# Performance work log

Measured on AMD Instinct MI355X. Metric: run time of the kernel, lower is better.

The kernel has to match this reference:

```python
import jax, jax.numpy as jnp
import numpy as np

HEADS = 16
DIM_HEAD = 64
SCALE = DIM_HEAD ** (-0.5)


def setup_inputs() -> dict:
    key = jax.random.key(0)
    ks = jax.random.split(key, 6)
    B, N, D = 2, 2048, 1024
    inner = HEADS * DIM_HEAD  # 1024
    s = 0.02
    return {
        "x": jax.random.normal(ks[0], (B, N, D), dtype=jnp.float32),
        "Wq": jax.random.normal(ks[1], (D, inner), dtype=jnp.float32) * s,
        "Wk": jax.random.normal(ks[2], (D, inner), dtype=jnp.float32) * s,
        "Wv": jax.random.normal(ks[3], (D, inner), dtype=jnp.float32) * s,
        "Wo": jax.random.normal(ks[4], (inner, D), dtype=jnp.float32) * s,
        "bo": jnp.zeros((D,), dtype=jnp.float32),
    }


def reference(x, Wq, Wk, Wv, Wo, bo):
    B, N, _ = x.shape
    # projections, split heads: [B, N, inner] -> [B, H, N, d]
    def split(t):
        return t.reshape(B, N, HEADS, DIM_HEAD).transpose(0, 2, 1, 3)
    q = split(x @ Wq)
    k = split(x @ Wk)  # self-attention: context = x
    v = split(x @ Wv)
    # scores [B, H, N, N], softmax over keys
    scores = jnp.einsum('bhid,bhjd->bhij', q, k) * SCALE
    attn = jax.nn.softmax(scores, axis=-1)
    out = jnp.einsum('bhij,bhjd->bhid', attn, v)
    out = out.transpose(0, 2, 1, 3).reshape(B, N, HEADS * DIM_HEAD)
    return out @ Wo + bo
```

## Files before the change

kernel.cpp:

```cpp
#include <hip/hip_runtime.h>
#include <hip/hip_bf16.h>
#include <stdint.h>

typedef unsigned short u16;
typedef __attribute__((ext_vector_type(8))) short bf16x8;
typedef __attribute__((ext_vector_type(4))) float f32x4;
typedef __attribute__((ext_vector_type(4))) unsigned int u32x4;

#define QSCALE 0.18033688011112042f

__device__ __forceinline__ u16 f2bf(float f) {
  return __builtin_bit_cast(u16, __float2bfloat16(f));
}

__device__ __forceinline__ uint32_t pkcvt(float a, float b) {
  return (uint32_t)f2bf(a) | ((uint32_t)f2bf(b) << 16);
}

__device__ __forceinline__ void gll16(const void* g, void* l) {
  __builtin_amdgcn_global_load_lds(
      (__attribute__((address_space(1))) void*)(uintptr_t)g,
      (__attribute__((address_space(3))) void*)l, 16, 0, 0);
}

__global__ void cvt_x_kernel(const float* __restrict__ x, u16* __restrict__ xb) {
  size_t i = (size_t)blockIdx.x * 256 + threadIdx.x;
  const float4* p = (const float4*)x + i * 2;
  float4 a = p[0], b = p[1];
  ushort4 lo, hi;
  lo.x = f2bf(a.x); lo.y = f2bf(a.y); lo.z = f2bf(a.z); lo.w = f2bf(a.w);
  hi.x = f2bf(b.x); hi.y = f2bf(b.y); hi.z = f2bf(b.z); hi.w = f2bf(b.w);
  ((ushort4*)xb)[i * 2]     = lo;
  ((ushort4*)xb)[i * 2 + 1] = hi;
}

__global__ void cvt_w_kernel(const float* __restrict__ Wq, const float* __restrict__ Wk,
                             const float* __restrict__ Wv, const float* __restrict__ Wo,
                             u16* __restrict__ Wqkvt, u16* __restrict__ Wot) {
  __shared__ float tile[32][33];
  const int z = blockIdx.z;
  const float* src = (z == 0) ? Wq : (z == 1) ? Wk : (z == 2) ? Wv : Wo;
  const float scale = (z == 0) ? QSCALE : 1.0f;
  u16* dst = (z == 3) ? Wot : (Wqkvt + (size_t)z * 1024 * 1024);
  const int n0 = blockIdx.x * 32, k0 = blockIdx.y * 32;
  const int tx = threadIdx.x, ty = threadIdx.y;
#pragma unroll
  for (int i = 0; i < 4; ++i)
    tile[ty * 4 + i][tx] = src[(size_t)(k0 + ty * 4 + i) * 1024 + n0 + tx];
  __syncthreads();
#pragma unroll
  for (int i = 0; i < 4; ++i)
    dst[(size_t)(n0 + ty * 4 + i) * 1024 + k0 + tx] = f2bf(tile[tx][ty * 4 + i] * scale);
}

__global__ __launch_bounds__(256)
void gemm_qkv_kernel(const u16* __restrict__ A, const u16* __restrict__ Bt,
                     u16* __restrict__ Qb, u16* __restrict__ Kb, u16* __restrict__ Vtb) {
  __shared__ __align__(16) u16 As[128 * 32];
  __shared__ __align__(16) u16 Bs[128 * 32];
  const int row0 = blockIdx.x * 128, col0 = blockIdx.y * 128;
  const int tid = threadIdx.x, lane = tid & 63, wid = tid >> 6;
  const int wr = (wid >> 1) * 64, wc = (wid & 1) * 64;
  const int lr = lane & 15, lk = (lane >> 4) * 8;

  f32x4 acc[4][4];
#pragma unroll
  for (int m = 0; m < 4; ++m)
#pragma unroll
    for (int n = 0; n < 4; ++n) acc[m][n] = (f32x4){0.f, 0.f, 0.f, 0.f};

  const int c0 = wid * 128 + lane;

  for (int k0 = 0; k0 < 1024; k0 += 32) {
    __syncthreads();
#pragma unroll
    for (int c = 0; c < 2; ++c) {
      const int chunk = c0 + c * 64;
      const int r = chunk >> 2, kk = (chunk & 3) * 8;
      gll16(A + (size_t)(row0 + r) * 1024 + k0 + kk,
            (char*)As + (wid * 128 + c * 64) * 16);
      gll16(Bt + (size_t)(col0 + r) * 1024 + k0 + kk,
            (char*)Bs + (wid * 128 + c * 64) * 16);
    }
    __syncthreads();
    bf16x8 af[4], bfr[4];
#pragma unroll
    for (int m = 0; m < 4; ++m)
      af[m] = *(const bf16x8*)&As[(wr + m * 16 + lr) * 32 + lk];
#pragma unroll
    for (int n = 0; n < 4; ++n)
      bfr[n] = *(const bf16x8*)&Bs[(wc + n * 16 + lr) * 32 + lk];
#pragma unroll
    for (int m = 0; m < 4; ++m)
#pragma unroll
      for (int n = 0; n < 4; ++n)
        acc[m][n] = __builtin_amdgcn_mfma_f32_16x16x32_bf16(af[m], bfr[n], acc[m][n], 0, 0, 0);
  }

  const int lg = lane >> 4;
#pragma unroll
  for (int m = 0; m < 4; ++m) {
#pragma unroll
    for (int n = 0; n < 4; ++n) {
      const int gcol = col0 + wc + n * 16 + lr;
      const int w = gcol >> 10, rem = gcol & 1023;
      const int h = rem >> 6, dd = rem & 63;
      const int grow0 = row0 + wr + m * 16 + lg * 4;
      if (w == 2) {
        const int b0 = grow0 >> 11, nn0 = grow0 & 2047;
        ushort4 sv;
        sv.x = f2bf(acc[m][n][0]); sv.y = f2bf(acc[m][n][1]);
        sv.z = f2bf(acc[m][n][2]); sv.w = f2bf(acc[m][n][3]);
        *(ushort4*)&Vtb[((size_t)(b0 * 16 + h) * 64 + dd) * 2048 + nn0] = sv;
      } else {
#pragma unroll
        for (int r = 0; r < 4; ++r) {
          const int grow = grow0 + r;
          const int b = grow >> 11, nn = grow & 2047;
          const int bh = b * 16 + h;
          const u16 hv = f2bf(acc[m][n][r]);
          if (w == 0) Qb[((size_t)bh * 2048 + nn) * 64 + dd] = hv;
          else        Kb[((size_t)bh * 2048 + nn) * 64 + dd] = hv;
        }
      }
    }
  }
}

__global__ __launch_bounds__(256, 2)
void attn_kernel(const u16* __restrict__ Qb, const u16* __restrict__ Kb,
                 const u16* __restrict__ Vtb, u16* __restrict__ Ob) {
  __shared__ __align__(16) u16 Ks[2][64 * 64];
  __shared__ __align__(16) u16 Vs[2][64 * 64];
  const int tid = threadIdx.x, lane = tid & 63, wid = tid >> 6;
  const int bid = blockIdx.x;
  const int vv = (bid & 7) * 64 + (bid >> 3);
  const int qt = vv & 15, bh = vv >> 4;
  const int lr = lane & 15, lg = lane >> 4;

  const u16* Qp = Qb + ((size_t)bh * 2048 + qt * 128 + wid * 32) * 64;
  const char* Kg = (const char*)(Kb + (size_t)bh * 2048 * 64);
  const char* Vg = (const char*)(Vtb + (size_t)bh * 64 * 2048);

  bf16x8 aq[2][2];
#pragma unroll
  for (int qc = 0; qc < 2; ++qc)
#pragma unroll
    for (int ks = 0; ks < 2; ++ks)
      aq[qc][ks] = *(const bf16x8*)&Qp[(qc * 16 + lr) * 64 + ks * 32 + lg * 8];

  const int c_base = wid * 128 + lane;
  auto stage = [&](int buf, int kv0) {
#pragma unroll
    for (int i = 0; i < 2; ++i) {
      const int c = c_base + i * 64;
      const int row = c >> 3;
      const int sc = ((c & 7) * 16) ^ ((row & 7) << 4);
      gll16(Kg + (size_t)(kv0 + row) * 128 + sc, (char*)Ks[buf] + c * 16);
      gll16(Vg + (size_t)row * 4096 + kv0 * 2 + sc, (char*)Vs[buf] + c * 16);
    }
  };

  const int swz = (lr & 7) << 4;
  const int xk0 = (lg * 16) ^ swz;
  const int xk1 = (64 + lg * 16) ^ swz;

  f32x4 acco[4][2];
#pragma unroll
  for (int ct = 0; ct < 4; ++ct)
#pragma unroll
    for (int qc = 0; qc < 2; ++qc) acco[ct][qc] = (f32x4){0.f, 0.f, 0.f, 0.f};
  f32x4 lacc[2];
  lacc[0] = (f32x4){0.f, 0.f, 0.f, 0.f};
  lacc[1] = (f32x4){0.f, 0.f, 0.f, 0.f};
  const f32x4 minit = (f32x4){-8.f, -8.f, -8.f, -8.f};
  u32x4 ow;
  ow.x = ow.y = ow.z = ow.w = 0x3F803F80u;
  const bf16x8 ones = __builtin_bit_cast(bf16x8, ow);

  stage(0, 0);
  asm volatile("s_waitcnt vmcnt(0)" ::: "memory");
  __syncthreads();

  int buf = 0;
  for (int t = 0; t < 32; ++t) {
    if (t < 31) stage(buf ^ 1, (t + 1) * 64);
    const char* kbase = (const char*)Ks[buf] + lr * 128;
    const char* vbase = (const char*)Vs[buf] + lr * 128;

    bf16x8 kf[4][2];
#pragma unroll
    for (int kt = 0; kt < 4; ++kt) {
      kf[kt][0] = *(const bf16x8*)(kbase + kt * 2048 + xk0);
      kf[kt][1] = *(const bf16x8*)(kbase + kt * 2048 + xk1);
    }
    f32x4 s[4][2];
#pragma unroll
    for (int kt = 0; kt < 4; ++kt)
#pragma unroll
      for (int qc = 0; qc < 2; ++qc) {
        f32x4 tacc = __builtin_amdgcn_mfma_f32_16x16x32_bf16(kf[kt][0], aq[qc][0], minit, 0, 0, 0);
        s[kt][qc]  = __builtin_amdgcn_mfma_f32_16x16x32_bf16(kf[kt][1], aq[qc][1], tacc, 0, 0, 0);
      }
    bf16x8 pa[2][2];
#pragma unroll
    for (int qc = 0; qc < 2; ++qc) {
#pragma unroll
      for (int kt = 0; kt < 4; ++kt)
#pragma unroll
        for (int r = 0; r < 4; ++r)
          s[kt][qc][r] = __builtin_amdgcn_exp2f(s[kt][qc][r]);
#pragma unroll
      for (int ks = 0; ks < 2; ++ks) {
        u32x4 w;
        w.x = pkcvt(s[2 * ks][qc][0],     s[2 * ks][qc][1]);
        w.y = pkcvt(s[2 * ks][qc][2],     s[2 * ks][qc][3]);
        w.z = pkcvt(s[2 * ks + 1][qc][0], s[2 * ks + 1][qc][1]);
        w.w = pkcvt(s[2 * ks + 1][qc][2], s[2 * ks + 1][qc][3]);
        pa[qc][ks] = __builtin_bit_cast(bf16x8, w);
      }
      lacc[qc] = __builtin_amdgcn_mfma_f32_16x16x32_bf16(ones, pa[qc][0], lacc[qc], 0, 0, 0);
      lacc[qc] = __builtin_amdgcn_mfma_f32_16x16x32_bf16(ones, pa[qc][1], lacc[qc], 0, 0, 0);
    }
#pragma unroll
    for (int ct = 0; ct < 4; ++ct) {
      const char* vb = vbase + ct * 2048;
#pragma unroll
      for (int ks = 0; ks < 2; ++ks) {
        uint2 lo = *(const uint2*)(vb + ((ks * 64 + lg * 8) ^ swz));
        uint2 hi = *(const uint2*)(vb + ((ks * 64 + 32 + lg * 8) ^ swz));
        u32x4 vw = {lo.x, lo.y, hi.x, hi.y};
        bf16x8 vf = __builtin_bit_cast(bf16x8, vw);
#pragma unroll
        for (int qc = 0; qc < 2; ++qc)
          acco[ct][qc] = __builtin_amdgcn_mfma_f32_16x16x32_bf16(vf, pa[qc][ks], acco[ct][qc], 0, 0, 0);
      }
    }
    asm volatile("s_waitcnt vmcnt(0)" ::: "memory");
    __syncthreads();
    buf ^= 1;
  }

  const int b = bh >> 4, h = bh & 15;
#pragma unroll
  for (int qc = 0; qc < 2; ++qc) {
    const int q = qt * 128 + wid * 32 + qc * 16 + lr;
    const float inv = 1.0f / lacc[qc][0];
#pragma unroll
    for (int ct = 0; ct < 4; ++ct) {
      uint2 st;
      st.x = pkcvt(acco[ct][qc][0] * inv, acco[ct][qc][1] * inv);
      st.y = pkcvt(acco[ct][qc][2] * inv, acco[ct][qc][3] * inv);
      *(uint2*)&Ob[((size_t)b * 2048 + q) * 1024 + h * 64 + ct * 16 + lg * 4] = st;
    }
  }
}

__global__ __launch_bounds__(256)
void gemm_out_kernel(const u16* __restrict__ A, const u16* __restrict__ Bt,
                     const float* __restrict__ bo, float* __restrict__ out) {
  __shared__ __align__(16) u16 As[128 * 32];
  __shared__ __align__(16) u16 Bs[128 * 32];
  const int row0 = blockIdx.x * 128, col0 = blockIdx.y * 128;
  const int tid = threadIdx.x, lane = tid & 63, wid = tid >> 6;
  const int wr = (wid >> 1) * 64, wc = (wid & 1) * 64;
  const int lr = lane & 15, lk = (lane >> 4) * 8;

  f32x4 acc[4][4];
#pragma unroll
  for (int m = 0; m < 4; ++m)
#pragma unroll
    for (int n = 0; n < 4; ++n) acc[m][n] = (f32x4){0.f, 0.f, 0.f, 0.f};

  const int c0 = wid * 128 + lane;

  for (int k0 = 0; k0 < 1024; k0 += 32) {
    __syncthreads();
#pragma unroll
    for (int c = 0; c < 2; ++c) {
      const int chunk = c0 + c * 64;
      const int r = chunk >> 2, kk = (chunk & 3) * 8;
      gll16(A + (size_t)(row0 + r) * 1024 + k0 + kk,
            (char*)As + (wid * 128 + c * 64) * 16);
      gll16(Bt + (size_t)(col0 + r) * 1024 + k0 + kk,
            (char*)Bs + (wid * 128 + c * 64) * 16);
    }
    __syncthreads();
    bf16x8 af[4], bfr[4];
#pragma unroll
    for (int m = 0; m < 4; ++m)
      af[m] = *(const bf16x8*)&As[(wr + m * 16 + lr) * 32 + lk];
#pragma unroll
    for (int n = 0; n < 4; ++n)
      bfr[n] = *(const bf16x8*)&Bs[(wc + n * 16 + lr) * 32 + lk];
#pragma unroll
    for (int m = 0; m < 4; ++m)
#pragma unroll
      for (int n = 0; n < 4; ++n)
        acc[m][n] = __builtin_amdgcn_mfma_f32_16x16x32_bf16(af[m], bfr[n], acc[m][n], 0, 0, 0);
  }

  const int lg = lane >> 4;
#pragma unroll
  for (int m = 0; m < 4; ++m) {
#pragma unroll
    for (int n = 0; n < 4; ++n) {
      const int gcol = col0 + wc + n * 16 + lr;
      const float bv = bo[gcol];
#pragma unroll
      for (int r = 0; r < 4; ++r) {
        const int grow = row0 + wr + m * 16 + lg * 4 + r;
        out[(size_t)grow * 1024 + gcol] = acc[m][n][r] + bv;
      }
    }
  }
}

extern "C" void kernel_launch(void* const* d_in, const int* in_sizes, int n_in,
                              void* d_out, int out_size, void* d_ws, size_t ws_size,
                              hipStream_t stream) {
  const float* x  = (const float*)d_in[0];
  const float* Wq = (const float*)d_in[1];
  const float* Wk = (const float*)d_in[2];
  const float* Wv = (const float*)d_in[3];
  const float* Wo = (const float*)d_in[4];
  const float* bo = (const float*)d_in[5];
  float* out = (float*)d_out;

  char* ws = (char*)d_ws;
  u16* xb    = (u16*)(ws);
  u16* wqkvt = (u16*)(ws + ((size_t)8  << 20));
  u16* wot   = (u16*)(ws + ((size_t)14 << 20));
  u16* Qb    = (u16*)(ws + ((size_t)16 << 20));
  u16* Kb    = (u16*)(ws + ((size_t)24 << 20));
  u16* Vtb   = (u16*)(ws + ((size_t)32 << 20));
  u16* Ob    = xb;

  hipLaunchKernelGGL(cvt_x_kernel, dim3(2048), dim3(256), 0, stream, x, xb);
  hipLaunchKernelGGL(cvt_w_kernel, dim3(32, 32, 4), dim3(32, 8), 0, stream,
                     Wq, Wk, Wv, Wo, wqkvt, wot);
  hipLaunchKernelGGL(gemm_qkv_kernel, dim3(32, 24), dim3(256), 0, stream,
                     xb, wqkvt, Qb, Kb, Vtb);
  hipLaunchKernelGGL(attn_kernel, dim3(512), dim3(256), 0, stream,
                     Qb, Kb, Vtb, Ob);
  hipLaunchKernelGGL(gemm_out_kernel, dim3(32, 8), dim3(256), 0, stream,
                     Ob, wot, bo, out);
}
```

Measured before the change: 121.8 us.

## Merge conversion kernels, permute V layout for 16-byte loads, add MFMA priority hints

Combines the x and weight conversion kernels into a single launch, saving one kernel dispatch. The V^T tensor is now written with a permuted key order inside each 64-key block, so the attention kernel can fetch each V fragment with one 16-byte LDS read instead of two 8-byte reads. s_setprio calls raise wave priority around the QK and PV MFMA sections so matrix work issues ahead of other waves. The permutation must match the P fragment layout exactly, otherwise results are wrong.

Measured after the change: 113.6 us. -6.7%, faster.

```diff
diff --git a/kernel.cpp b/kernel.cpp
--- a/kernel.cpp
+++ b/kernel.cpp
@@ -23,34 +23,37 @@
       (__attribute__((address_space(3))) void*)l, 16, 0, 0);
 }
 
-__global__ void cvt_x_kernel(const float* __restrict__ x, u16* __restrict__ xb) {
-  size_t i = (size_t)blockIdx.x * 256 + threadIdx.x;
-  const float4* p = (const float4*)x + i * 2;
-  float4 a = p[0], b = p[1];
-  ushort4 lo, hi;
-  lo.x = f2bf(a.x); lo.y = f2bf(a.y); lo.z = f2bf(a.z); lo.w = f2bf(a.w);
-  hi.x = f2bf(b.x); hi.y = f2bf(b.y); hi.z = f2bf(b.z); hi.w = f2bf(b.w);
-  ((ushort4*)xb)[i * 2]     = lo;
-  ((ushort4*)xb)[i * 2 + 1] = hi;
-}
-
-__global__ void cvt_w_kernel(const float* __restrict__ Wq, const float* __restrict__ Wk,
-                             const float* __restrict__ Wv, const float* __restrict__ Wo,
-                             u16* __restrict__ Wqkvt, u16* __restrict__ Wot) {
+__global__ __launch_bounds__(256)
+void cvt_all_kernel(const float* __restrict__ x,
+                    const float* __restrict__ Wq, const float* __restrict__ Wk,
+                    const float* __restrict__ Wv, const float* __restrict__ Wo,
+                    u16* __restrict__ xb, u16* __restrict__ Wqkvt, u16* __restrict__ Wot) {
   __shared__ float tile[32][33];
-  const int z = blockIdx.z;
-  const float* src = (z == 0) ? Wq : (z == 1) ? Wk : (z == 2) ? Wv : Wo;
-  const float scale = (z == 0) ? QSCALE : 1.0f;
-  u16* dst = (z == 3) ? Wot : (Wqkvt + (size_t)z * 1024 * 1024);
-  const int n0 = blockIdx.x * 32, k0 = blockIdx.y * 32;
-  const int tx = threadIdx.x, ty = threadIdx.y;
-#pragma unroll
-  for (int i = 0; i < 4; ++i)
-    tile[ty * 4 + i][tx] = src[(size_t)(k0 + ty * 4 + i) * 1024 + n0 + tx];
-  __syncthreads();
-#pragma unroll
-  for (int i = 0; i < 4; ++i)
-    dst[(size_t)(n0 + ty * 4 + i) * 1024 + k0 + tx] = f2bf(tile[tx][ty * 4 + i] * scale);
+  const int bid = blockIdx.x, tid = threadIdx.x;
+  if (bid < 4096) {
+    const int z = bid >> 10, xy = bid & 1023;
+    const float* src = (z == 0) ? Wq : (z == 1) ? Wk : (z == 2) ? Wv : Wo;
+    const float scale = (z == 0) ? QSCALE : 1.0f;
+    u16* dst = (z == 3) ? Wot : (Wqkvt + (size_t)z * 1024 * 1024);
+    const int n0 = (xy & 31) * 32, k0 = (xy >> 5) * 32;
+    const int tx = tid & 31, ty = tid >> 5;
+#pragma unroll
+    for (int i = 0; i < 4; ++i)
+      tile[ty * 4 + i][tx] = src[(size_t)(k0 + ty * 4 + i) * 1024 + n0 + tx];
+    __syncthreads();
+#pragma unroll
+    for (int i = 0; i < 4; ++i)
+      dst[(size_t)(n0 + ty * 4 + i) * 1024 + k0 + tx] = f2bf(tile[tx][ty * 4 + i] * scale);
+  } else {
+    size_t i = (size_t)(bid - 4096) * 256 + tid;
+    const float4* p = (const float4*)x + i * 2;
+    float4 a = p[0], b = p[1];
+    ushort4 lo, hi;
+    lo.x = f2bf(a.x); lo.y = f2bf(a.y); lo.z = f2bf(a.z); lo.w = f2bf(a.w);
+    hi.x = f2bf(b.x); hi.y = f2bf(b.y); hi.z = f2bf(b.z); hi.w = f2bf(b.w);
+    ((ushort4*)xb)[i * 2]     = lo;
+    ((ushort4*)xb)[i * 2 + 1] = hi;
+  }
 }
 
 __global__ __launch_bounds__(256)
@@ -108,10 +111,12 @@
       const int grow0 = row0 + wr + m * 16 + lg * 4;
       if (w == 2) {
         const int b0 = grow0 >> 11, nn0 = grow0 & 2047;
+        const int kin = nn0 & 63;
+        const int kp = (kin & 32) | ((kin & 12) << 1) | ((kin & 16) >> 2);
         ushort4 sv;
         sv.x = f2bf(acc[m][n][0]); sv.y = f2bf(acc[m][n][1]);
         sv.z = f2bf(acc[m][n][2]); sv.w = f2bf(acc[m][n][3]);
-        *(ushort4*)&Vtb[((size_t)(b0 * 16 + h) * 64 + dd) * 2048 + nn0] = sv;
+        *(ushort4*)&Vtb[((size_t)(b0 * 16 + h) * 64 + dd) * 2048 + (nn0 & ~63) + kp] = sv;
       } else {
 #pragma unroll
         for (int r = 0; r < 4; ++r) {
@@ -195,6 +200,7 @@
       kf[kt][1] = *(const bf16x8*)(kbase + kt * 2048 + xk1);
     }
     f32x4 s[4][2];
+    __builtin_amdgcn_s_setprio(1);
 #pragma unroll
     for (int kt = 0; kt < 4; ++kt)
 #pragma unroll
@@ -202,6 +208,7 @@
         f32x4 tacc = __builtin_amdgcn_mfma_f32_16x16x32_bf16(kf[kt][0], aq[qc][0], minit, 0, 0, 0);
         s[kt][qc]  = __builtin_amdgcn_mfma_f32_16x16x32_bf16(kf[kt][1], aq[qc][1], tacc, 0, 0, 0);
       }
+    __builtin_amdgcn_s_setprio(0);
     bf16x8 pa[2][2];
 #pragma unroll
     for (int qc = 0; qc < 2; ++qc) {
@@ -222,20 +229,19 @@
       lacc[qc] = __builtin_amdgcn_mfma_f32_16x16x32_bf16(ones, pa[qc][0], lacc[qc], 0, 0, 0);
       lacc[qc] = __builtin_amdgcn_mfma_f32_16x16x32_bf16(ones, pa[qc][1], lacc[qc], 0, 0, 0);
     }
+    __builtin_amdgcn_s_setprio(1);
 #pragma unroll
     for (int ct = 0; ct < 4; ++ct) {
       const char* vb = vbase + ct * 2048;
 #pragma unroll
       for (int ks = 0; ks < 2; ++ks) {
-        uint2 lo = *(const uint2*)(vb + ((ks * 64 + lg * 8) ^ swz));
-        uint2 hi = *(const uint2*)(vb + ((ks * 64 + 32 + lg * 8) ^ swz));
-        u32x4 vw = {lo.x, lo.y, hi.x, hi.y};
-        bf16x8 vf = __builtin_bit_cast(bf16x8, vw);
+        bf16x8 vf = *(const bf16x8*)(vb + ((ks * 64 + lg * 16) ^ swz));
 #pragma unroll
         for (int qc = 0; qc < 2; ++qc)
           acco[ct][qc] = __builtin_amdgcn_mfma_f32_16x16x32_bf16(vf, pa[qc][ks], acco[ct][qc], 0, 0, 0);
       }
     }
+    __builtin_amdgcn_s_setprio(0);
     asm volatile("s_waitcnt vmcnt(0)" ::: "memory");
     __syncthreads();
     buf ^= 1;
@@ -336,9 +342,8 @@
   u16* Vtb   = (u16*)(ws + ((size_t)32 << 20));
   u16* Ob    = xb;
 
-  hipLaunchKernelGGL(cvt_x_kernel, dim3(2048), dim3(256), 0, stream, x, xb);
-  hipLaunchKernelGGL(cvt_w_kernel, dim3(32, 32, 4), dim3(32, 8), 0, stream,
-                     Wq, Wk, Wv, Wo, wqkvt, wot);
+  hipLaunchKernelGGL(cvt_all_kernel, dim3(6144), dim3(256), 0, stream,
+                     x, Wq, Wk, Wv, Wo, xb, wqkvt, wot);
   hipLaunchKernelGGL(gemm_qkv_kernel, dim3(32, 24), dim3(256), 0, stream,
                      xb, wqkvt, Qb, Kb, Vtb);
   hipLaunchKernelGGL(attn_kernel, dim3(512), dim3(256), 0, stream,
```
